# Kernel tuning notes

Hardware: AMD Instinct MI355X
Metric: run time of the kernel (lower is better)

Reference implementation:

```python
import jax, jax.numpy as jnp
import numpy as np

B, N, C, M, OUT = 4, 256, 32, 4, 64


def _uniform(k, shape, fan_in):
    s = 1.0 / np.sqrt(fan_in)
    return jax.random.uniform(k, shape, jnp.float32, -s, s)


def setup_inputs() -> dict:
    key = jax.random.key(0)
    ks = jax.random.split(key, 11)
    return {
        "x": jax.random.normal(ks[0], (B, N, N, C), jnp.float32),
        # Neighborhood / SnConv2to1 linears (in=C, out=M neighborhood channels)
        "w1_nb": _uniform(ks[1], (3 * C, M), 3 * C),
        "b1_nb": _uniform(ks[2], (M,), 3 * C),
        "w0_nb": _uniform(ks[3], (2 * C, M), 2 * C),
        "b0_nb": _uniform(ks[4], (M,), 2 * C),
        # SnConv2 linears (in channels = M*C after neighborhood product)
        "w2d": _uniform(ks[5], (2 * M * C, OUT), 2 * M * C),
        "b2d": _uniform(ks[6], (OUT,), 2 * M * C),
        "w1d": _uniform(ks[7], (3 * M * C, OUT), 3 * M * C),
        "b1d": _uniform(ks[8], (OUT,), 3 * M * C),
        "w0d": _uniform(ks[9], (2 * M * C, OUT), 2 * M * C),
        "b0d": _uniform(ks[10], (OUT,), 2 * M * C),
    }


def _contractions(x):
    # x: [B, n, n, c]; mask=None, reduction='mean' path of _get_contractions
    n = x.shape[1]
    rowsum = x.sum(axis=1) / n                      # [B, n, c]
    colsum = x.sum(axis=2) / n                      # [B, n, c]
    diag = jnp.diagonal(x, axis1=1, axis2=2)        # [B, c, n]
    rowcolsum = x.sum(axis=(1, 2)) / (n * n)        # [B, c]
    diag_sum = diag.sum(axis=-1) / n                # [B, c]  (/= sqrt(n^2))
    diag = jnp.moveaxis(diag, -1, 1)                # move_from_end -> [B, n, c]
    return rowsum, colsum, diag, rowcolsum, diag_sum


def reference(x, w1_nb, b1_nb, w0_nb, b0_nb, w2d, b2d, w1d, b1d, w0d, b0d):
    # ---- Neighborhood: SnConv2to1 -> sigmoid ----
    rs, cs, dg, rcs, ds = _contractions(x)
    obj1 = jnp.concatenate([rs, cs, dg], axis=-1)             # [B, n, 3C]
    obj0 = jnp.concatenate([rcs, ds], axis=-1)                # [B, 2C]
    node = obj1 @ w1_nb + b1_nb + (obj0 @ w0_nb + b0_nb)[:, None, :]
    neighbs = jax.nn.sigmoid(node)                            # [B, n, M]
    # ---- _neighbor_elementwise_product ----
    expanded = neighbs[:, None, :, :] * neighbs[:, :, None, :]  # [B, n, n, M]
    # channel_product: outer product over channel dims, collapsed to M*C
    xl = (expanded[..., :, None] * x[..., None, :]).reshape(B, N, N, M * C)
    # ---- SnConv2 on the localized tensor ----
    rs2, cs2, dg2, rcs2, ds2 = _contractions(xl)
    obj2d = jnp.concatenate([xl, jnp.swapaxes(xl, 1, 2)], axis=-1)  # [B,n,n,2MC]
    obj1d = jnp.concatenate([rs2, cs2, dg2], axis=-1)               # [B,n,3MC]
    obj0d = jnp.concatenate([rcs2, ds2], axis=-1)                   # [B,2MC]
    out = (obj2d @ w2d + b2d
           + (obj1d @ w1d + b1d)[:, None, :, :]
           + (obj0d @ w0d + b0d)[:, None, None, :])                 # [B,n,n,OUT]
    return out
```

## Files before the change

kernel.cpp:

```cpp
#include <hip/hip_runtime.h>
#include <math.h>

#define Bv 4
#define Nv 256
#define Cv 32
#define Mv 4
#define OUTv 64
#define MCv (Mv*Cv)

typedef _Float16 h8 __attribute__((ext_vector_type(8)));
typedef _Float16 h4 __attribute__((ext_vector_type(4)));
typedef float f4 __attribute__((ext_vector_type(4)));

__device__ __align__(16) float g_rs  [Bv * Nv * Cv];
__device__ __align__(16) float g_cs  [Bv * Nv * Cv];
__device__ __align__(16) float g_dgx [Bv * Nv * Cv];
__device__ __align__(16) float g_nb  [Bv * Nv * Mv];
__device__ __align__(16) float g_S1  [Bv * Nv * MCv];
__device__ __align__(16) float g_S2  [Bv * Nv * MCv];
__device__ __align__(16) float g_rcs2[Bv * MCv];
__device__ __align__(16) float g_ds2 [Bv * MCv];
__device__ __align__(16) float g_t0g [Bv * OUTv];
__device__ __align__(16) float g_addv[Bv * Nv * OUTv];
__device__ __align__(16) _Float16 g_wfrag[8 * 4 * 64 * 8];

__global__ void k_wpack(const float* __restrict__ w2d) {
    int t = threadIdx.x;
    int r = blockIdx.x;
    int fi = r * 256 + t;
    int s = fi >> 8, q = (fi >> 6) & 3, lane = fi & 63;
    int k0 = s * 32 + ((lane >> 4) << 3);
    int o = q * 16 + (lane & 15);
    #pragma unroll
    for (int jj = 0; jj < 8; jj++)
        g_wfrag[fi * 8 + jj] = (_Float16)w2d[(size_t)(k0 + jj) * OUTv + o];
}

__global__ void k_contract1(const float* __restrict__ x) {
    int n = blockIdx.x, b = blockIdx.y;
    int t = threadIdx.x, c4 = t & 7, sub = t >> 3;
    const float4* xb4 = (const float4*)(x + (size_t)b * Nv * Nv * Cv);
    float4 aC = {0.f,0.f,0.f,0.f}, aR = {0.f,0.f,0.f,0.f};
    for (int j = sub; j < Nv; j += 32) {
        float4 v = xb4[(n * Nv + j) * 8 + c4];
        aC.x += v.x; aC.y += v.y; aC.z += v.z; aC.w += v.w;
    }
    for (int i = sub; i < Nv; i += 32) {
        float4 v = xb4[(i * Nv + n) * 8 + c4];
        aR.x += v.x; aR.y += v.y; aR.z += v.z; aR.w += v.w;
    }
    __shared__ float red[2][32][36];
    red[0][sub][c4*4+0] = aC.x; red[0][sub][c4*4+1] = aC.y;
    red[0][sub][c4*4+2] = aC.z; red[0][sub][c4*4+3] = aC.w;
    red[1][sub][c4*4+0] = aR.x; red[1][sub][c4*4+1] = aR.y;
    red[1][sub][c4*4+2] = aR.z; red[1][sub][c4*4+3] = aR.w;
    __syncthreads();
    if (t < 64) {
        int which = t >> 5, c = t & 31;
        float s = 0.f;
        #pragma unroll
        for (int k = 0; k < 32; k++) s += red[which][k][c];
        s *= (1.0f / Nv);
        if (which == 0) g_cs[(b * Nv + n) * Cv + c] = s;
        else            g_rs[(b * Nv + n) * Cv + c] = s;
    }
    if (t < 8) ((float4*)g_dgx)[(b * Nv + n) * 8 + t] = xb4[(n * Nv + n) * 8 + t];
}

__global__ void k_neighb(const float* __restrict__ w1, const float* __restrict__ b1,
                         const float* __restrict__ w0, const float* __restrict__ b0) {
    int b = blockIdx.x, t = threadIdx.x;
    if (t < MCv) {
        g_rcs2[b * MCv + t] = 0.f;
        g_ds2 [b * MCv + t] = 0.f;
    }
    int c = t & 31, sub = t >> 5;
    float ar = 0.f, ad = 0.f;
    for (int n = sub; n < Nv; n += 8) {
        ar += g_rs[(b * Nv + n) * Cv + c];
        ad += g_dgx[(b * Nv + n) * Cv + c];
    }
    __shared__ float red[8][64];
    __shared__ float obj0[64];
    __shared__ float t0nb[4];
    red[sub][c] = ar;
    red[sub][32 + c] = ad;
    __syncthreads();
    if (t < 64) {
        float s = 0.f;
        #pragma unroll
        for (int k = 0; k < 8; k++) s += red[k][t];
        obj0[t] = s * (1.0f / Nv);
    }
    __syncthreads();
    if (t < 4) {
        float v = b0[t];
        for (int k = 0; k < 2 * Cv; k++) v += obj0[k] * w0[k * Mv + t];
        t0nb[t] = v;
    }
    __syncthreads();
    int n = t;
    float node[4];
    #pragma unroll
    for (int m = 0; m < 4; m++) node[m] = t0nb[m] + b1[m];
    for (int cc = 0; cc < Cv; cc++) {
        float r = g_rs[(b * Nv + n) * Cv + cc];
        float s = g_cs[(b * Nv + n) * Cv + cc];
        float d = g_dgx[(b * Nv + n) * Cv + cc];
        #pragma unroll
        for (int m = 0; m < 4; m++)
            node[m] += r * w1[cc * Mv + m] + s * w1[(Cv + cc) * Mv + m] + d * w1[(2 * Cv + cc) * Mv + m];
    }
    #pragma unroll
    for (int m = 0; m < 4; m++)
        g_nb[(b * Nv + n) * Mv + m] = 1.0f / (1.0f + expf(-node[m]));
}

__global__ void k_wsum(const float* __restrict__ x) {
    int n = blockIdx.x, b = blockIdx.y;
    int t = threadIdx.x, c4 = t & 7, sub = t >> 3;
    __shared__ __align__(16) float4 nbl[Nv];
    if (t < Nv) nbl[t] = ((const float4*)(g_nb + (size_t)b * Nv * Mv))[t];
    __syncthreads();
    const float4* xb4 = (const float4*)(x + (size_t)b * Nv * Nv * Cv);
    float4 a2[4], a1[4];
    #pragma unroll
    for (int m = 0; m < 4; m++) { a2[m] = {0.f,0.f,0.f,0.f}; a1[m] = {0.f,0.f,0.f,0.f}; }
    for (int j = sub; j < Nv; j += 32) {
        float4 v = xb4[(n * Nv + j) * 8 + c4];
        float4 nv = nbl[j];
        a2[0].x += nv.x*v.x; a2[0].y += nv.x*v.y; a2[0].z += nv.x*v.z; a2[0].w += nv.x*v.w;
        a2[1].x += nv.y*v.x; a2[1].y += nv.y*v.y; a2[1].z += nv.y*v.z; a2[1].w += nv.y*v.w;
        a2[2].x += nv.z*v.x; a2[2].y += nv.z*v.y; a2[2].z += nv.z*v.z; a2[2].w += nv.z*v.w;
        a2[3].x += nv.w*v.x; a2[3].y += nv.w*v.y; a2[3].z += nv.w*v.z; a2[3].w += nv.w*v.w;
    }
    for (int i = sub; i < Nv; i += 32) {
        float4 v = xb4[(i * Nv + n) * 8 + c4];
        float4 nv = nbl[i];
        a1[0].x += nv.x*v.x; a1[0].y += nv.x*v.y; a1[0].z += nv.x*v.z; a1[0].w += nv.x*v.w;
        a1[1].x += nv.y*v.x; a1[1].y += nv.y*v.y; a1[1].z += nv.y*v.z; a1[1].w += nv.y*v.w;
        a1[2].x += nv.z*v.x; a1[2].y += nv.z*v.y; a1[2].z += nv.z*v.z; a1[2].w += nv.z*v.w;
        a1[3].x += nv.w*v.x; a1[3].y += nv.w*v.y; a1[3].z += nv.w*v.z; a1[3].w += nv.w*v.w;
    }
    __shared__ float red[32][132];
    #pragma unroll
    for (int m = 0; m < 4; m++) {
        red[sub][m*32 + c4*4+0] = a2[m].x; red[sub][m*32 + c4*4+1] = a2[m].y;
        red[sub][m*32 + c4*4+2] = a2[m].z; red[sub][m*32 + c4*4+3] = a2[m].w;
    }
    __syncthreads();
    if (t < 128) {
        float s = 0.f;
        #pragma unroll
        for (int k = 0; k < 32; k++) s += red[k][t];
        g_S2[(size_t)(b * Nv + n) * MCv + t] = s;
    }
    __syncthreads();
    #pragma unroll
    for (int m = 0; m < 4; m++) {
        red[sub][m*32 + c4*4+0] = a1[m].x; red[sub][m*32 + c4*4+1] = a1[m].y;
        red[sub][m*32 + c4*4+2] = a1[m].z; red[sub][m*32 + c4*4+3] = a1[m].w;
    }
    __syncthreads();
    if (t < 128) {
        float s = 0.f;
        #pragma unroll
        for (int k = 0; k < 32; k++) s += red[k][t];
        g_S1[(size_t)(b * Nv + n) * MCv + t] = s;
        int m = t >> 5, c = t & 31;
        float nv = ((const float*)&nbl[n])[m];
        atomicAdd(&g_rcs2[b * MCv + t], nv * s);
        atomicAdd(&g_ds2 [b * MCv + t], nv * nv * g_dgx[(b * Nv + n) * Cv + c]);
    }
}

__global__ void k_t0(const float* __restrict__ w0d, const float* __restrict__ b0d) {
    int b = blockIdx.x, t = threadIdx.x;
    __shared__ float rc[MCv], ds[MCv];
    rc[t] = g_rcs2[b * MCv + t] * (1.0f / ((float)Nv * Nv));
    ds[t] = g_ds2 [b * MCv + t] * (1.0f / Nv);
    __syncthreads();
    if (t < OUTv) {
        float v = b0d[t];
        for (int k = 0; k < MCv; k++)
            v += rc[k] * w0d[k * OUTv + t] + ds[k] * w0d[(MCv + k) * OUTv + t];
        g_t0g[b * OUTv + t] = v;
    }
}

__global__ void k_add(const float* __restrict__ w1d, const float* __restrict__ b1d,
                      const float* __restrict__ b2d) {
    int b = blockIdx.y;
    int n = blockIdx.x * 4 + (threadIdx.x >> 6);
    int o = threadIdx.x & 63;
    float acc = b1d[o] + b2d[o] + g_t0g[b * OUTv + o];
    const float invN = 1.0f / Nv;
    #pragma unroll
    for (int m = 0; m < 4; m++) {
        float nv = g_nb[(b * Nv + n) * Mv + m];
        float f = nv * invN, d2 = nv * nv;
        for (int c = 0; c < Cv; c++) {
            int mc = m * Cv + c;
            acc += f * g_S1[(size_t)(b * Nv + n) * MCv + mc] * w1d[mc * OUTv + o]
                 + f * g_S2[(size_t)(b * Nv + n) * MCv + mc] * w1d[(MCv + mc) * OUTv + o]
                 + d2 * g_dgx[(b * Nv + n) * Cv + c] * w1d[(2 * MCv + mc) * OUTv + o];
        }
    }
    g_addv[(size_t)(b * Nv + n) * OUTv + o] = acc;
}

#define XPAD 40
__global__ __launch_bounds__(256) void k_main(const float* __restrict__ x,
                                              float* __restrict__ out) {
    int jt = blockIdx.x, i = blockIdx.y, b = blockIdx.z;
    int j0 = jt * 128;
    int t = threadIdx.x;
    int lane = t & 63, w = t >> 6;
    int rowA = lane & 15, quad = lane >> 4;

    __shared__ __align__(16) _Float16 Wl[8 * 4 * 64 * 8];
    __shared__ __align__(16) _Float16 Xt[128 * XPAD];
    __shared__ __align__(16) _Float16 Xb[128 * XPAD];

    {
        const float4* src = (const float4*)g_wfrag;
        float4* dst = (float4*)Wl;
        #pragma unroll
        for (int r = 0; r < 8; r++) dst[r * 256 + t] = src[r * 256 + t];
    }
    {
        const float4* x4 = (const float4*)x;
        #pragma unroll
        for (int r = 0; r < 4; r++) {
            int idx = r * 256 + t;
            int j = idx >> 3, c4 = idx & 7;
            float4 v = x4[((size_t)(b * Nv + i) * Nv + j0 + j) * 8 + c4];
            h4 hv; hv[0] = (_Float16)v.x; hv[1] = (_Float16)v.y;
            hv[2] = (_Float16)v.z; hv[3] = (_Float16)v.w;
            *(h4*)&Xt[j * XPAD + c4 * 4] = hv;
            float4 u = x4[((size_t)(b * Nv + j0 + j) * Nv + i) * 8 + c4];
            h4 hu; hu[0] = (_Float16)u.x; hu[1] = (_Float16)u.y;
            hu[2] = (_Float16)u.z; hu[3] = (_Float16)u.w;
            *(h4*)&Xb[j * XPAD + c4 * 4] = hu;
        }
    }
    int jl1 = w * 32 + rowA, jl2 = jl1 + 16;
    _Float16 e1h[4], e2h[4];
    {
        const float* ni = g_nb + (size_t)(b * Nv + i) * Mv;
        const float* n1 = g_nb + (size_t)(b * Nv + j0 + jl1) * Mv;
        const float* n2 = g_nb + (size_t)(b * Nv + j0 + jl2) * Mv;
        #pragma unroll
        for (int m = 0; m < 4; m++) {
            e1h[m] = (_Float16)(ni[m] * n1[m]);
            e2h[m] = (_Float16)(ni[m] * n2[m]);
        }
    }
    __syncthreads();

    f4 acc[2][4];
    #pragma unroll
    for (int js = 0; js < 2; js++)
        #pragma unroll
        for (int q = 0; q < 4; q++) acc[js][q] = {0.f, 0.f, 0.f, 0.f};

    const h8* Wf = (const h8*)Wl;
    #pragma unroll
    for (int part = 0; part < 2; part++) {
        const _Float16* X = part ? Xb : Xt;
        h8 xv1 = *(const h8*)&X[jl1 * XPAD + quad * 8];
        h8 xv2 = *(const h8*)&X[jl2 * XPAD + quad * 8];
        #pragma unroll
        for (int m = 0; m < 4; m++) {
            h8 a1 = xv1 * e1h[m];
            h8 a2 = xv2 * e2h[m];
            int s = part * 4 + m;
            #pragma unroll
            for (int q = 0; q < 4; q++) {
                h8 bf = Wf[(s * 4 + q) * 64 + lane];
                acc[0][q] = __builtin_amdgcn_mfma_f32_16x16x32_f16(a1, bf, acc[0][q], 0, 0, 0);
                acc[1][q] = __builtin_amdgcn_mfma_f32_16x16x32_f16(a2, bf, acc[1][q], 0, 0, 0);
            }
        }
    }
    #pragma unroll
    for (int js = 0; js < 2; js++) {
        int jbase = j0 + w * 32 + js * 16 + quad * 4;
        #pragma unroll
        for (int q = 0; q < 4; q++) {
            int o = q * 16 + rowA;
            #pragma unroll
            for (int r = 0; r < 4; r++) {
                int j = jbase + r;
                float v = acc[js][q][r] + g_addv[(size_t)(b * Nv + j) * OUTv + o];
                out[(((size_t)(b * Nv + i)) * Nv + j) * OUTv + o] = v;
            }
        }
    }
}

extern "C" void kernel_launch(void* const* d_in, const int* in_sizes, int n_in,
                              void* d_out, int out_size, void* d_ws, size_t ws_size,
                              hipStream_t stream) {
    const float* x     = (const float*)d_in[0];
    const float* w1_nb = (const float*)d_in[1];
    const float* b1_nb = (const float*)d_in[2];
    const float* w0_nb = (const float*)d_in[3];
    const float* b0_nb = (const float*)d_in[4];
    const float* w2d   = (const float*)d_in[5];
    const float* b2d   = (const float*)d_in[6];
    const float* w1d   = (const float*)d_in[7];
    const float* b1d   = (const float*)d_in[8];
    const float* w0d   = (const float*)d_in[9];
    const float* b0d   = (const float*)d_in[10];
    float* out = (float*)d_out;
    (void)d_ws; (void)ws_size;

    hipLaunchKernelGGL(k_wpack, dim3(8), dim3(256), 0, stream, w2d);
    hipLaunchKernelGGL(k_contract1, dim3(Nv, Bv), dim3(256), 0, stream, x);
    hipLaunchKernelGGL(k_neighb, dim3(Bv), dim3(256), 0, stream,
                       w1_nb, b1_nb, w0_nb, b0_nb);
    hipLaunchKernelGGL(k_wsum, dim3(Nv, Bv), dim3(256), 0, stream, x);
    hipLaunchKernelGGL(k_t0, dim3(Bv), dim3(128), 0, stream, w0d, b0d);
    hipLaunchKernelGGL(k_add, dim3(Nv / 4, Bv), dim3(256), 0, stream,
                       w1d, b1d, b2d);
    hipLaunchKernelGGL(k_main, dim3(2, Nv, Bv), dim3(256), 0, stream, x, out);
}
```

Baseline: 186.2 us.

## Restructure row/column reduction passes into tiled blocks with split work

Replaces the per-node contraction and weighted-sum kernels with tiled versions. Half the blocks handle eight columns over all rows and the other half handle eight rows, so each block covers contiguous 8-row or 8-column tiles instead of one node's strided row and column. The diagonal is captured during the column pass, and zeroing the atomic accumulators moves into the weight-pack kernel. This cuts the grid from 256 to 64 blocks per batch. The intent is better memory coalescing and fewer blocks, at the risk of lower parallelism and more atomics per block.

Result: slower. 248.4 us (+33.4%).

```diff
diff --git a/kernel.cpp b/kernel.cpp
--- a/kernel.cpp
+++ b/kernel.cpp
@@ -24,9 +24,14 @@
 __device__ __align__(16) float g_addv[Bv * Nv * OUTv];
 __device__ __align__(16) _Float16 g_wfrag[8 * 4 * 64 * 8];
 
-__global__ void k_wpack(const float* __restrict__ w2d) {
+__global__ void k_wpackz(const float* __restrict__ w2d) {
     int t = threadIdx.x;
     int r = blockIdx.x;
+    if (r == 8) {
+        if (t < 128) ((float4*)g_rcs2)[t] = {0.f,0.f,0.f,0.f};
+        else         ((float4*)g_ds2)[t - 128] = {0.f,0.f,0.f,0.f};
+        return;
+    }
     int fi = r * 256 + t;
     int s = fi >> 8, q = (fi >> 6) & 3, lane = fi & 63;
     int k0 = s * 32 + ((lane >> 4) << 3);
@@ -36,44 +41,65 @@
         g_wfrag[fi * 8 + jj] = (_Float16)w2d[(size_t)(k0 + jj) * OUTv + o];
 }
 
-__global__ void k_contract1(const float* __restrict__ x) {
-    int n = blockIdx.x, b = blockIdx.y;
-    int t = threadIdx.x, c4 = t & 7, sub = t >> 3;
-    const float4* xb4 = (const float4*)(x + (size_t)b * Nv * Nv * Cv);
-    float4 aC = {0.f,0.f,0.f,0.f}, aR = {0.f,0.f,0.f,0.f};
-    for (int j = sub; j < Nv; j += 32) {
-        float4 v = xb4[(n * Nv + j) * 8 + c4];
-        aC.x += v.x; aC.y += v.y; aC.z += v.z; aC.w += v.w;
-    }
-    for (int i = sub; i < Nv; i += 32) {
-        float4 v = xb4[(i * Nv + n) * 8 + c4];
-        aR.x += v.x; aR.y += v.y; aR.z += v.z; aR.w += v.w;
-    }
-    __shared__ float red[2][32][36];
-    red[0][sub][c4*4+0] = aC.x; red[0][sub][c4*4+1] = aC.y;
-    red[0][sub][c4*4+2] = aC.z; red[0][sub][c4*4+3] = aC.w;
-    red[1][sub][c4*4+0] = aR.x; red[1][sub][c4*4+1] = aR.y;
-    red[1][sub][c4*4+2] = aR.z; red[1][sub][c4*4+3] = aR.w;
-    __syncthreads();
-    if (t < 64) {
-        int which = t >> 5, c = t & 31;
-        float s = 0.f;
-        #pragma unroll
-        for (int k = 0; k < 32; k++) s += red[which][k][c];
-        s *= (1.0f / Nv);
-        if (which == 0) g_cs[(b * Nv + n) * Cv + c] = s;
-        else            g_rs[(b * Nv + n) * Cv + c] = s;
-    }
-    if (t < 8) ((float4*)g_dgx)[(b * Nv + n) * 8 + t] = xb4[(n * Nv + n) * 8 + t];
+__global__ __launch_bounds__(256) void k_passA(const float* __restrict__ x) {
+    int b = blockIdx.y;
+    const float4* x4 = (const float4*)(x + (size_t)b * Nv * Nv * Cv);
+    int t = threadIdx.x;
+    __shared__ __align__(16) float4 red[256];
+    if (blockIdx.x < 32) {
+        int j0 = blockIdx.x * 8;
+        int isub = t >> 6, jc = (t >> 3) & 7, c4 = t & 7;
+        int jrow = j0 + jc;
+        float4 acc = {0.f,0.f,0.f,0.f};
+        for (int i = isub; i < Nv; i += 4) {
+            float4 v = x4[((size_t)i * Nv + jrow) * 8 + c4];
+            acc.x += v.x; acc.y += v.y; acc.z += v.z; acc.w += v.w;
+            if (i == jrow) ((float4*)g_dgx)[(b * Nv + i) * 8 + c4] = v;
+        }
+        red[t] = acc;
+        __syncthreads();
+        if (t < 64) {
+            float4 s = red[t];
+            #pragma unroll
+            for (int k = 1; k < 4; k++) {
+                float4 v = red[k * 64 + t];
+                s.x += v.x; s.y += v.y; s.z += v.z; s.w += v.w;
+            }
+            const float sc = 1.0f / Nv;
+            s.x *= sc; s.y *= sc; s.z *= sc; s.w *= sc;
+            int jc2 = t >> 3, c42 = t & 7;
+            ((float4*)g_rs)[(b * Nv + j0 + jc2) * 8 + c42] = s;
+        }
+    } else {
+        int i0 = (blockIdx.x - 32) * 8;
+        int ic = t >> 5, jsub = (t >> 3) & 3, c4 = t & 7;
+        int irow = i0 + ic;
+        float4 acc = {0.f,0.f,0.f,0.f};
+        for (int jj = 0; jj < 64; jj++) {
+            int j = jsub + jj * 4;
+            float4 v = x4[((size_t)irow * Nv + j) * 8 + c4];
+            acc.x += v.x; acc.y += v.y; acc.z += v.z; acc.w += v.w;
+        }
+        red[t] = acc;
+        __syncthreads();
+        if (t < 64) {
+            int ic2 = t >> 3, c42 = t & 7;
+            float4 s = {0.f,0.f,0.f,0.f};
+            #pragma unroll
+            for (int k = 0; k < 4; k++) {
+                float4 v = red[ic2 * 32 + k * 8 + c42];
+                s.x += v.x; s.y += v.y; s.z += v.z; s.w += v.w;
+            }
+            const float sc = 1.0f / Nv;
+            s.x *= sc; s.y *= sc; s.z *= sc; s.w *= sc;
+            ((float4*)g_cs)[(b * Nv + i0 + ic2) * 8 + c42] = s;
+        }
+    }
 }
 
 __global__ void k_neighb(const float* __restrict__ w1, const float* __restrict__ b1,
                          const float* __restrict__ w0, const float* __restrict__ b0) {
     int b = blockIdx.x, t = threadIdx.x;
-    if (t < MCv) {
-        g_rcs2[b * MCv + t] = 0.f;
-        g_ds2 [b * MCv + t] = 0.f;
-    }
     int c = t & 31, sub = t >> 5;
     float ar = 0.f, ad = 0.f;
     for (int n = sub; n < Nv; n += 8) {
@@ -116,61 +142,96 @@
         g_nb[(b * Nv + n) * Mv + m] = 1.0f / (1.0f + expf(-node[m]));
 }
 
-__global__ void k_wsum(const float* __restrict__ x) {
-    int n = blockIdx.x, b = blockIdx.y;
-    int t = threadIdx.x, c4 = t & 7, sub = t >> 3;
-    __shared__ __align__(16) float4 nbl[Nv];
-    if (t < Nv) nbl[t] = ((const float4*)(g_nb + (size_t)b * Nv * Mv))[t];
-    __syncthreads();
-    const float4* xb4 = (const float4*)(x + (size_t)b * Nv * Nv * Cv);
-    float4 a2[4], a1[4];
-    #pragma unroll
-    for (int m = 0; m < 4; m++) { a2[m] = {0.f,0.f,0.f,0.f}; a1[m] = {0.f,0.f,0.f,0.f}; }
-    for (int j = sub; j < Nv; j += 32) {
-        float4 v = xb4[(n * Nv + j) * 8 + c4];
-        float4 nv = nbl[j];
-        a2[0].x += nv.x*v.x; a2[0].y += nv.x*v.y; a2[0].z += nv.x*v.z; a2[0].w += nv.x*v.w;
-        a2[1].x += nv.y*v.x; a2[1].y += nv.y*v.y; a2[1].z += nv.y*v.z; a2[1].w += nv.y*v.w;
-        a2[2].x += nv.z*v.x; a2[2].y += nv.z*v.y; a2[2].z += nv.z*v.z; a2[2].w += nv.z*v.w;
-        a2[3].x += nv.w*v.x; a2[3].y += nv.w*v.y; a2[3].z += nv.w*v.z; a2[3].w += nv.w*v.w;
-    }
-    for (int i = sub; i < Nv; i += 32) {
-        float4 v = xb4[(i * Nv + n) * 8 + c4];
-        float4 nv = nbl[i];
-        a1[0].x += nv.x*v.x; a1[0].y += nv.x*v.y; a1[0].z += nv.x*v.z; a1[0].w += nv.x*v.w;
-        a1[1].x += nv.y*v.x; a1[1].y += nv.y*v.y; a1[1].z += nv.y*v.z; a1[1].w += nv.y*v.w;
-        a1[2].x += nv.z*v.x; a1[2].y += nv.z*v.y; a1[2].z += nv.z*v.z; a1[2].w += nv.z*v.w;
-        a1[3].x += nv.w*v.x; a1[3].y += nv.w*v.y; a1[3].z += nv.w*v.z; a1[3].w += nv.w*v.w;
-    }
-    __shared__ float red[32][132];
-    #pragma unroll
-    for (int m = 0; m < 4; m++) {
-        red[sub][m*32 + c4*4+0] = a2[m].x; red[sub][m*32 + c4*4+1] = a2[m].y;
-        red[sub][m*32 + c4*4+2] = a2[m].z; red[sub][m*32 + c4*4+3] = a2[m].w;
-    }
-    __syncthreads();
-    if (t < 128) {
-        float s = 0.f;
-        #pragma unroll
-        for (int k = 0; k < 32; k++) s += red[k][t];
-        g_S2[(size_t)(b * Nv + n) * MCv + t] = s;
-    }
-    __syncthreads();
-    #pragma unroll
-    for (int m = 0; m < 4; m++) {
-        red[sub][m*32 + c4*4+0] = a1[m].x; red[sub][m*32 + c4*4+1] = a1[m].y;
-        red[sub][m*32 + c4*4+2] = a1[m].z; red[sub][m*32 + c4*4+3] = a1[m].w;
-    }
-    __syncthreads();
-    if (t < 128) {
-        float s = 0.f;
-        #pragma unroll
-        for (int k = 0; k < 32; k++) s += red[k][t];
-        g_S1[(size_t)(b * Nv + n) * MCv + t] = s;
-        int m = t >> 5, c = t & 31;
-        float nv = ((const float*)&nbl[n])[m];
-        atomicAdd(&g_rcs2[b * MCv + t], nv * s);
-        atomicAdd(&g_ds2 [b * MCv + t], nv * nv * g_dgx[(b * Nv + n) * Cv + c]);
+__global__ __launch_bounds__(256) void k_passB(const float* __restrict__ x) {
+    int b = blockIdx.y;
+    int t = threadIdx.x;
+    __shared__ __align__(16) float nbs[Nv * Mv];
+    __shared__ __align__(16) float4 red[4 * 256];
+    ((float4*)nbs)[t] = ((const float4*)(g_nb + (size_t)b * Nv * Mv))[t];
+    __syncthreads();
+    const float4* x4 = (const float4*)(x + (size_t)b * Nv * Nv * Cv);
+    if (blockIdx.x < 32) {
+        int j0 = blockIdx.x * 8;
+        int isub = t >> 6, jc = (t >> 3) & 7, c4 = t & 7;
+        int jrow = j0 + jc;
+        float4 acc[4];
+        #pragma unroll
+        for (int m = 0; m < 4; m++) acc[m] = {0.f,0.f,0.f,0.f};
+        float4 diagv = {0.f,0.f,0.f,0.f};
+        for (int i = isub; i < Nv; i += 4) {
+            float4 v = x4[((size_t)i * Nv + jrow) * 8 + c4];
+            float4 w = *(const float4*)&nbs[i * 4];
+            acc[0].x += w.x*v.x; acc[0].y += w.x*v.y; acc[0].z += w.x*v.z; acc[0].w += w.x*v.w;
+            acc[1].x += w.y*v.x; acc[1].y += w.y*v.y; acc[1].z += w.y*v.z; acc[1].w += w.y*v.w;
+            acc[2].x += w.z*v.x; acc[2].y += w.z*v.y; acc[2].z += w.z*v.z; acc[2].w += w.z*v.w;
+            acc[3].x += w.w*v.x; acc[3].y += w.w*v.y; acc[3].z += w.w*v.z; acc[3].w += w.w*v.w;
+            if (i == jrow) diagv = v;
+        }
+        #pragma unroll
+        for (int m = 0; m < 4; m++) red[m * 256 + t] = acc[m];
+        __syncthreads();
+        if (t < 64) {
+            int jc2 = t >> 3, c42 = t & 7;
+            int n = j0 + jc2;
+            #pragma unroll
+            for (int m = 0; m < 4; m++) {
+                float4 s = red[m * 256 + t];
+                #pragma unroll
+                for (int k = 1; k < 4; k++) {
+                    float4 v = red[m * 256 + k * 64 + t];
+                    s.x += v.x; s.y += v.y; s.z += v.z; s.w += v.w;
+                }
+                ((float4*)g_S1)[((size_t)(b * Nv + n)) * 32 + m * 8 + c42] = s;
+                float nv = nbs[n * 4 + m];
+                atomicAdd(&g_rcs2[b * MCv + m * 32 + c42 * 4 + 0], nv * s.x);
+                atomicAdd(&g_rcs2[b * MCv + m * 32 + c42 * 4 + 1], nv * s.y);
+                atomicAdd(&g_rcs2[b * MCv + m * 32 + c42 * 4 + 2], nv * s.z);
+                atomicAdd(&g_rcs2[b * MCv + m * 32 + c42 * 4 + 3], nv * s.w);
+            }
+        }
+        if ((jrow & 3) == isub) {
+            #pragma unroll
+            for (int m = 0; m < 4; m++) {
+                float nv = nbs[jrow * 4 + m];
+                float w2 = nv * nv;
+                atomicAdd(&g_ds2[b * MCv + m * 32 + c4 * 4 + 0], w2 * diagv.x);
+                atomicAdd(&g_ds2[b * MCv + m * 32 + c4 * 4 + 1], w2 * diagv.y);
+                atomicAdd(&g_ds2[b * MCv + m * 32 + c4 * 4 + 2], w2 * diagv.z);
+                atomicAdd(&g_ds2[b * MCv + m * 32 + c4 * 4 + 3], w2 * diagv.w);
+            }
+        }
+    } else {
+        int i0 = (blockIdx.x - 32) * 8;
+        int ic = t >> 5, jsub = (t >> 3) & 3, c4 = t & 7;
+        int irow = i0 + ic;
+        float4 acc[4];
+        #pragma unroll
+        for (int m = 0; m < 4; m++) acc[m] = {0.f,0.f,0.f,0.f};
+        for (int jj = 0; jj < 64; jj++) {
+            int j = jsub + jj * 4;
+            float4 v = x4[((size_t)irow * Nv + j) * 8 + c4];
+            float4 w = *(const float4*)&nbs[j * 4];
+            acc[0].x += w.x*v.x; acc[0].y += w.x*v.y; acc[0].z += w.x*v.z; acc[0].w += w.x*v.w;
+            acc[1].x += w.y*v.x; acc[1].y += w.y*v.y; acc[1].z += w.y*v.z; acc[1].w += w.y*v.w;
+            acc[2].x += w.z*v.x; acc[2].y += w.z*v.y; acc[2].z += w.z*v.z; acc[2].w += w.z*v.w;
+            acc[3].x += w.w*v.x; acc[3].y += w.w*v.y; acc[3].z += w.w*v.z; acc[3].w += w.w*v.w;
+        }
+        #pragma unroll
+        for (int m = 0; m < 4; m++) red[m * 256 + t] = acc[m];
+        __syncthreads();
+        if (t < 64) {
+            int ic2 = t >> 3, c42 = t & 7;
+            #pragma unroll
+            for (int m = 0; m < 4; m++) {
+                float4 s = {0.f,0.f,0.f,0.f};
+                #pragma unroll
+                for (int k = 0; k < 4; k++) {
+                    float4 v = red[m * 256 + ic2 * 32 + k * 8 + c42];
+                    s.x += v.x; s.y += v.y; s.z += v.z; s.w += v.w;
+                }
+                ((float4*)g_S2)[((size_t)(b * Nv + i0 + ic2)) * 32 + m * 8 + c42] = s;
+            }
+        }
     }
 }
 
@@ -316,11 +377,11 @@
     float* out = (float*)d_out;
     (void)d_ws; (void)ws_size;
 
-    hipLaunchKernelGGL(k_wpack, dim3(8), dim3(256), 0, stream, w2d);
-    hipLaunchKernelGGL(k_contract1, dim3(Nv, Bv), dim3(256), 0, stream, x);
+    hipLaunchKernelGGL(k_wpackz, dim3(9), dim3(256), 0, stream, w2d);
+    hipLaunchKernelGGL(k_passA, dim3(64, Bv), dim3(256), 0, stream, x);
     hipLaunchKernelGGL(k_neighb, dim3(Bv), dim3(256), 0, stream,
                        w1_nb, b1_nb, w0_nb, b0_nb);
-    hipLaunchKernelGGL(k_wsum, dim3(Nv, Bv), dim3(256), 0, stream, x);
+    hipLaunchKernelGGL(k_passB, dim3(64, Bv), dim3(256), 0, stream, x);
     hipLaunchKernelGGL(k_t0, dim3(Bv), dim3(128), 0, stream, w0d, b0d);
     hipLaunchKernelGGL(k_add, dim3(Nv / 4, Bv), dim3(256), 0, stream,
                        w1d, b1d, b2d);
```
